# Performance work log

Hardware: AMD Instinct MI355X
Metric: run time of the kernel (lower is better)

The kernel has to match this reference:

```python
import jax, jax.numpy as jnp
import numpy as np

B = 8                                   # point clouds per batch
NS = [65536, 16384, 4096, 1024, 256]    # points per scale (stride-4 downsampling)
CS = [32, 64, 128, 256, 512]            # encoder channels per scale
K = 3
BN_EPS = 1e-5


def setup_inputs() -> dict:
    key = jax.random.key(0)
    ks = iter(jax.random.split(key, 64))
    inp = {}
    for i, (n, c) in enumerate(zip(NS, CS)):
        inp[f"p{i}"] = jax.random.uniform(next(ks), (n, 3), jnp.float32)
        inp[f"f{i}"] = jax.random.normal(next(ks), (n, c), jnp.float32)
        inp[f"b{i}"] = jnp.repeat(jnp.arange(B, dtype=jnp.int32), n // B)
    # FP stage mlps: a:(4->3) [768,256,256], b:(3->2) [384,128,128],
    #               c:(2->1) [192,64,64],   d:(1->0) [96,32,32]
    cfg = {"a": (CS[3] + CS[4], CS[3]), "b": (CS[2] + CS[3], CS[2]),
           "c": (CS[1] + CS[2], CS[1]), "d": (CS[0] + CS[1], CS[0])}
    for s, (cin, ch) in cfg.items():
        for j, ci in ((1, cin), (2, ch)):
            inp[f"w{s}{j}"] = jax.random.normal(next(ks), (ci, ch), jnp.float32) / float(np.sqrt(ci))
            inp[f"bias{s}{j}"] = jnp.zeros((ch,), jnp.float32)
            inp[f"g{s}{j}"] = jnp.ones((ch,), jnp.float32)
            inp[f"bt{s}{j}"] = jnp.zeros((ch,), jnp.float32)
    return inp


def _knn_interpolate(x2, p2, p1):
    """torch_geometric.nn.knn_interpolate with k=3; equal-sized sorted batches."""
    n1, n2, c = p1.shape[0] // B, p2.shape[0] // B, x2.shape[1]
    p1b, p2b = p1.reshape(B, n1, 3), p2.reshape(B, n2, 3)
    x2b = x2.reshape(B, n2, c)
    # squared dists via |a|^2 + |b|^2 - 2ab (avoids [B,n1,n2,3] temporary)
    d2 = (jnp.sum(p1b * p1b, -1)[:, :, None] + jnp.sum(p2b * p2b, -1)[:, None, :]
          - 2.0 * jnp.einsum('bnd,bmd->bnm', p1b, p2b))
    neg_d2, idx = jax.lax.top_k(-d2, K)              # [B, n1, K]
    w = 1.0 / jnp.maximum(-neg_d2, 1e-16)            # inverse squared distance
    gath = jax.vmap(lambda x, i: x[i])(x2b, idx)     # [B, n1, K, c]
    out = jnp.einsum('bnk,bnkc->bnc', w, gath) / jnp.sum(w, -1, keepdims=True)
    return out.reshape(B * n1, c)


def _lin_bn_relu(x, w, bias, gamma, beta):
    h = x @ w + bias
    mu = jnp.mean(h, 0)
    var = jnp.mean((h - mu) ** 2, 0)
    return jax.nn.relu((h - mu) * jax.lax.rsqrt(var + BN_EPS) * gamma + beta)


def _fp_stage(p_fine, f_fine, p_coarse, f_coarse, w1, b1, g1, bt1, w2, b2, g2, bt2):
    up = _knn_interpolate(f_coarse, p_coarse, p_fine)
    x = jnp.concatenate([f_fine, up], axis=1)
    x = _lin_bn_relu(x, w1, b1, g1, bt1)
    return _lin_bn_relu(x, w2, b2, g2, bt2)


def reference(p0, p1, p2, p3, p4, f0, f1, f2, f3, f4, b0, b1, b2, b3, b4,
              wa1, biasa1, ga1, bta1, wa2, biasa2, ga2, bta2,
              wb1, biasb1, gb1, btb1, wb2, biasb2, gb2, btb2,
              wc1, biasc1, gc1, btc1, wc2, biasc2, gc2, btc2,
              wd1, biasd1, gd1, btd1, wd2, biasd2, gd2, btd2):
    f3 = _fp_stage(p3, f3, p4, f4, wa1, biasa1, ga1, bta1, wa2, biasa2, ga2, bta2)
    f2 = _fp_stage(p2, f2, p3, f3, wb1, biasb1, gb1, btb1, wb2, biasb2, gb2, btb2)
    f1 = _fp_stage(p1, f1, p2, f2, wc1, biasc1, gc1, btc1, wc2, biasc2, gc2, btc2)
    f0 = _fp_stage(p0, f0, p1, f1, wd1, biasd1, gd1, btd1, wd2, biasd2, gd2, btd2)
    return f0
```

## Files before the change

### kernel.cpp

```cpp
#include <hip/hip_runtime.h>

#define BN_EPS 1e-5f

typedef unsigned short us;

__device__ __forceinline__ float bf2f(us u) {
    union { unsigned int i; float f; } v; v.i = ((unsigned int)u) << 16; return v.f;
}
__device__ __forceinline__ us f2bf(float f) {
    unsigned int x = __float_as_uint(f);
    x += 0x7fffu + ((x >> 16) & 1u);
    return (us)(x >> 16);
}
__device__ __forceinline__ float ldf(const void* p, size_t i, int f32) {
    return f32 ? ((const float*)p)[i] : bf2f(((const us*)p)[i]);
}

__global__ void detect_kernel(const unsigned int* __restrict__ g, int* __restrict__ flag) {
    if (threadIdx.x == 0 && blockIdx.x == 0)
        *flag = ((g[0] & 0xFFFFu) == 0u) ? 1 : 0;
}

__global__ __launch_bounds__(256)
void prep_aos_kernel(const void* __restrict__ p, float4* __restrict__ aos,
                     const int* __restrict__ pf32, int n)
{
    const int i = blockIdx.x * 256 + threadIdx.x;
    if (i >= n) return;
    const int f32 = *pf32;
    const float x = ldf(p, (size_t)3 * i + 0, f32);
    const float y = ldf(p, (size_t)3 * i + 1, f32);
    const float z = ldf(p, (size_t)3 * i + 2, f32);
    const float s2 = __fadd_rn(__fadd_rn(__fmul_rn(x, x), __fmul_rn(y, y)), __fmul_rn(z, z));
    aos[i] = make_float4(__fadd_rn(x, x), __fadd_rn(y, y), __fadd_rn(z, z), s2);
}

template<int NPB>
__global__ __launch_bounds__(NPB / 2)
void sort_aos_kernel(const void* __restrict__ p, const int* __restrict__ pf32,
                     float4* __restrict__ srt, int* __restrict__ jout)
{
    __shared__ float sk[NPB];
    __shared__ int   sj[NPB];
    const int f32 = *pf32;
    const int tid = threadIdx.x;
    const int base = blockIdx.x * NPB;
    for (int i = tid; i < NPB; i += NPB / 2) {
        sk[i] = ldf(p, (size_t)3 * (base + i) + 0, f32);
        sj[i] = i;
    }
    __syncthreads();
    for (int k = 2; k <= NPB; k <<= 1) {
        for (int j = k >> 1; j > 0; j >>= 1) {
            const int i = ((tid / j) * (j << 1)) + (tid % j);
            const int ixj = i + j;
            const bool up = ((i & k) == 0);
            const float a = sk[i], b = sk[ixj];
            const bool sw = up ? (a > b) : (a < b);
            if (sw) {
                sk[i] = b; sk[ixj] = a;
                const int t = sj[i]; sj[i] = sj[ixj]; sj[ixj] = t;
            }
            __syncthreads();
        }
    }
    for (int i = tid; i < NPB; i += NPB / 2) {
        const int jl = sj[i];
        const size_t b = (size_t)3 * (base + jl);
        const float x = ldf(p, b + 0, f32);
        const float y = ldf(p, b + 1, f32);
        const float z = ldf(p, b + 2, f32);
        const float s2 = __fadd_rn(__fadd_rn(__fmul_rn(x, x), __fmul_rn(y, y)),
                                   __fmul_rn(z, z));
        srt[base + i] = make_float4(__fadd_rn(x, x), __fadd_rn(y, y), __fadd_rn(z, z), s2);
        jout[base + i] = base + jl;
    }
}

__device__ __forceinline__ void lexmerge33(
    const float a0, const int A0, const float a1, const int A1, const float a2, const int A2,
    const float b0, const int B0, const float b1, const int B1, const float b2, const int B2,
    float& m0, int& M0, float& m1, int& M1, float& m2, int& M2)
{
    const bool c1 = (a0 < b0) || (a0 == b0 && A0 < B0);
    m0 = c1 ? a0 : b0;  M0 = c1 ? A0 : B0;
    const float hAd = c1 ? a1 : a0;  const int hAi = c1 ? A1 : A0;
    const float hBd = c1 ? b0 : b1;  const int hBi = c1 ? B0 : B1;
    const bool c2 = (hAd < hBd) || (hAd == hBd && hAi < hBi);
    m1 = c2 ? hAd : hBd;  M1 = c2 ? hAi : hBi;
    const float gAd = c2 ? (c1 ? a2 : a1) : hAd;  const int gAi = c2 ? (c1 ? A2 : A1) : hAi;
    const float gBd = c2 ? hBd : (c1 ? b1 : b2);  const int gBi = c2 ? hBi : (c1 ? B1 : B2);
    const bool c3 = (gAd < gBd) || (gAd == gBd && gAi < gBi);
    m2 = c3 ? gAd : gBd;  M2 = c3 ? gAi : gBi;
}

template<int NPB, int C2>
__global__ __launch_bounds__(256)
void knn_win_kernel(const void* __restrict__ p_fine,
                    const float4* __restrict__ srt,
                    const int* __restrict__ jsrt,
                    const float* __restrict__ f_coarse,
                    const float* __restrict__ stats,
                    const void* __restrict__ gamma,
                    const void* __restrict__ beta,
                    float inv_n2,
                    float* __restrict__ up_out,
                    const int* __restrict__ pf32)
{
    __shared__ __align__(16) float4 sA[NPB];
    __shared__ int   sJ[NPB];
    __shared__ float mrg_d[4 * 64 * 3];
    __shared__ int   mrg_i[4 * 64 * 3];
    __shared__ int   s_idx[64][3];
    __shared__ float s_w[64][3];
    __shared__ float aff_a[C2], aff_b[C2];

    const int f32 = *pf32;
    const int tid = threadIdx.x;
    const int lane = tid & 63, wv = tid >> 6;
    const int cb = blockIdx.y * NPB;
    const int row0 = (blockIdx.y * gridDim.x + blockIdx.x) * 64;

    for (int i = tid; i < NPB; i += 256) { sA[i] = srt[cb + i]; sJ[i] = jsrt[cb + i]; }
    for (int c = tid; c < C2; c += 256) {
        const float mu  = stats[c] * inv_n2;
        const float var = stats[C2 + c] * inv_n2 - mu * mu;
        const float a = ldf(gamma, c, f32) * rsqrtf(var + BN_EPS);
        aff_a[c] = a;
        aff_b[c] = ldf(beta, c, f32) - mu * a;
    }
    __syncthreads();

    const int row = row0 + lane;
    const size_t pb = (size_t)row * 3;
    const float px = ldf(p_fine, pb + 0, f32);
    const float py = ldf(p_fine, pb + 1, f32);
    const float pz = ldf(p_fine, pb + 2, f32);
    const float s1 = __fadd_rn(__fadd_rn(__fmul_rn(px, px), __fmul_rn(py, py)),
                               __fmul_rn(pz, pz));
    const float px2 = __fadd_rn(px, px);

    int lo = 0, hi = NPB;
    while (lo < hi) {
        const int mid = (lo + hi) >> 1;
        if (sA[mid].x < px2) lo = mid + 1; else hi = mid;
    }
    const int cpos = lo;

    float t0 = 1e30f, t1 = 1e30f, t2 = 1e30f;
    int i0 = 0, i1 = 0, i2 = 0;

#define WINS(A, D, JJ) {                                                      \
    const bool l0 = (A) && ((D) < t0 || ((D) == t0 && (JJ) < i0));            \
    const bool l1 = (A) && ((D) < t1 || ((D) == t1 && (JJ) < i1));            \
    const bool l2 = (A) && ((D) < t2 || ((D) == t2 && (JJ) < i2));            \
    i2 = l1 ? i1 : (l2 ? (JJ) : i2);                                          \
    i1 = l0 ? i0 : (l1 ? (JJ) : i1);                                          \
    i0 = l0 ? (JJ) : i0;                                                      \
    const float q2 = l1 ? t1 : (l2 ? (D) : t2);                               \
    const float q1 = l0 ? t0 : (l1 ? (D) : t1);                               \
    t0 = l0 ? (D) : t0;  t1 = q1;  t2 = q2; }

    {
        int pos = cpos + wv;
        bool alive = true;
        for (int it = 0; it < NPB / 4 + 2; ++it) {
            if (!__any(alive)) break;
            const bool inb = (pos < NPB);
            const int rp = inb ? pos : (NPB - 1);
            const float4 C = sA[rp];
            const float dq = __fsub_rn(px2, C.x);
            const float dq2 = __fmul_rn(dq, dq);
            alive = alive && inb && !(dq2 > fmaf(4.0f, t2, 4e-5f));
            const float dot2 = fmaf(pz, C.z, fmaf(py, C.y, __fmul_rn(px, C.x)));
            const float d = __fsub_rn(__fadd_rn(s1, C.w), dot2);
            const int jj = sJ[rp];
            WINS(alive, d, jj);
            pos += 4;
        }
    }
    {
        int pos = cpos - 1 - wv;
        bool alive = true;
        for (int it = 0; it < NPB / 4 + 2; ++it) {
            if (!__any(alive)) break;
            const bool inb = (pos >= 0);
            const int rp = inb ? pos : 0;
            const float4 C = sA[rp];
            const float dq = __fsub_rn(px2, C.x);
            const float dq2 = __fmul_rn(dq, dq);
            alive = alive && inb && !(dq2 > fmaf(4.0f, t2, 4e-5f));
            const float dot2 = fmaf(pz, C.z, fmaf(py, C.y, __fmul_rn(px, C.x)));
            const float d = __fsub_rn(__fadd_rn(s1, C.w), dot2);
            const int jj = sJ[rp];
            WINS(alive, d, jj);
            pos -= 4;
        }
    }
#undef WINS

    const int mb = (wv * 64 + lane) * 3;
    mrg_d[mb + 0] = t0;  mrg_i[mb + 0] = i0;
    mrg_d[mb + 1] = t1;  mrg_i[mb + 1] = i1;
    mrg_d[mb + 2] = t2;  mrg_i[mb + 2] = i2;
    __syncthreads();

    if (tid < 64) {
        float d0 = mrg_d[tid * 3 + 0], d1 = mrg_d[tid * 3 + 1], d2 = mrg_d[tid * 3 + 2];
        int   j0 = mrg_i[tid * 3 + 0], j1 = mrg_i[tid * 3 + 1], j2 = mrg_i[tid * 3 + 2];
        #pragma unroll
        for (int w = 1; w < 4; ++w) {
            const int b2 = (w * 64 + tid) * 3;
            float n0, n1, n2v; int ni0, ni1, ni2;
            lexmerge33(d0, j0, d1, j1, d2, j2,
                       mrg_d[b2 + 0], mrg_i[b2 + 0], mrg_d[b2 + 1], mrg_i[b2 + 1],
                       mrg_d[b2 + 2], mrg_i[b2 + 2],
                       n0, ni0, n1, ni1, n2v, ni2);
            d0 = n0; j0 = ni0; d1 = n1; j1 = ni1; d2 = n2v; j2 = ni2;
        }
        s_idx[tid][0] = j0;  s_w[tid][0] = __fdiv_rn(1.0f, fmaxf(d0, 1e-16f));
        s_idx[tid][1] = j1;  s_w[tid][1] = __fdiv_rn(1.0f, fmaxf(d1, 1e-16f));
        s_idx[tid][2] = j2;  s_w[tid][2] = __fdiv_rn(1.0f, fmaxf(d2, 1e-16f));
    }
    __syncthreads();

    for (int p = wv; p < 64; p += 4) {
        const int r2 = row0 + p;
        const int g0 = s_idx[p][0], g1 = s_idx[p][1], g2 = s_idx[p][2];
        const float w0 = s_w[p][0], w1 = s_w[p][1], w2 = s_w[p][2];
        const float den = __fadd_rn(__fadd_rn(w0, w1), w2);
        float* __restrict__ urow = up_out + (size_t)r2 * C2;
        for (int c = lane; c < C2; c += 64) {
            const float aa = aff_a[c], bb = aff_b[c];
            const float v0 = fmaxf(aa * f_coarse[(size_t)g0 * C2 + c] + bb, 0.f);
            const float v1 = fmaxf(aa * f_coarse[(size_t)g1 * C2 + c] + bb, 0.f);
            const float v2 = fmaxf(aa * f_coarse[(size_t)g2 * C2 + c] + bb, 0.f);
            const float num = fmaf(w2, v2, fmaf(w1, v1, __fmul_rn(w0, v0)));
            urow[c] = __fdiv_rn(num, den);
        }
    }
}

template<int MODE, int SPLIT, int LEN>
__global__ __launch_bounds__(64 * SPLIT, 8)
void knn_up_kernel(
    const void* __restrict__ p_fine,
    const float4* __restrict__ aos,
    const void* __restrict__ f_coarse,
    const float* __restrict__ stats,
    const void* __restrict__ gamma,
    const void* __restrict__ beta,
    float inv_n2,
    float* __restrict__ up_out,
    const int* __restrict__ pf32,
    int n2pb, int c2)
{
    __shared__ float mrg_d[SPLIT * 64 * 3];
    __shared__ int   mrg_i[SPLIT * 64 * 3];
    __shared__ float aff_a[256], aff_b[256];
    __shared__ int   s_idx[64][3];
    __shared__ float s_w[64][3];

    const int f32 = *pf32;
    const int tid = threadIdx.x;
    const int lane = tid & 63;
    const int wv = tid >> 6;
    const int cbase = blockIdx.y * n2pb;
    const int row0 = (blockIdx.y * gridDim.x + blockIdx.x) * 64;

    if (MODE == 1) {
        for (int c = tid; c < c2; c += 64 * SPLIT) {
            float mu  = stats[c] * inv_n2;
            float var = stats[c2 + c] * inv_n2 - mu * mu;
            float a = ldf(gamma, c, f32) * rsqrtf(var + BN_EPS);
            aff_a[c] = a;
            aff_b[c] = ldf(beta, c, f32) - mu * a;
        }
    }

    {
        const int row = row0 + lane;
        const size_t b = (size_t)row * 3;
        const float px = ldf(p_fine, b + 0, f32);
        const float py = ldf(p_fine, b + 1, f32);
        const float pz = ldf(p_fine, b + 2, f32);
        const float s1 = __fadd_rn(__fadd_rn(__fmul_rn(px, px), __fmul_rn(py, py)),
                                   __fmul_rn(pz, pz));
        const int jb = wv * LEN;
        unsigned long long spv = (unsigned long long)(const void*)(aos + cbase + jb);
        spv = ((unsigned long long)__builtin_amdgcn_readfirstlane((unsigned int)(spv >> 32)) << 32)
            |  (unsigned long long)__builtin_amdgcn_readfirstlane((unsigned int)spv);
        const float4* __restrict__ sl = (const float4*)spv;

        float t0 = 1e30f, t1 = 1e30f, t2 = 1e30f;
        int i0 = jb, i1 = jb, i2 = jb;

#define KNN_UPD(CQ, JJ) {                                                     \
        const float dot2 = fmaf(pz, (CQ).z, fmaf(py, (CQ).y,                  \
                                __fmul_rn(px, (CQ).x)));                      \
        const float d = __fsub_rn(__fadd_rn(s1, (CQ).w), dot2);               \
        const int jj = (JJ);                                                  \
        const bool a0 = d < t0, a1 = d < t1, a2 = d < t2;                     \
        i2 = a1 ? i1 : (a2 ? jj : i2);                                        \
        i1 = a0 ? i0 : (a1 ? jj : i1);                                        \
        i0 = a0 ? jj : i0;                                                    \
        const float nt1 = __builtin_amdgcn_fmed3f(d, t0, t1);                 \
        const float nt2 = __builtin_amdgcn_fmed3f(d, t1, t2);                 \
        t0 = fminf(d, t0);                                                    \
        t1 = nt1; t2 = nt2; }

        float4 ca = sl[0], cb = sl[1], cc = sl[2], cd = sl[3];
        for (int t = 0; t < LEN; t += 4) {
            float4 na, nb, nc, nd;
            const bool more = (t + 4) < LEN;
            if (more) { na = sl[t + 4]; nb = sl[t + 5]; nc = sl[t + 6]; nd = sl[t + 7]; }
            KNN_UPD(ca, jb + t + 0);
            KNN_UPD(cb, jb + t + 1);
            KNN_UPD(cc, jb + t + 2);
            KNN_UPD(cd, jb + t + 3);
            if (more) { ca = na; cb = nb; cc = nc; cd = nd; }
        }
#undef KNN_UPD

        const int mb = (wv * 64 + lane) * 3;
        mrg_d[mb + 0] = t0;  mrg_i[mb + 0] = cbase + i0;
        mrg_d[mb + 1] = t1;  mrg_i[mb + 1] = cbase + i1;
        mrg_d[mb + 2] = t2;  mrg_i[mb + 2] = cbase + i2;
    }
    __syncthreads();

    if (tid < 64) {
        float d0 = mrg_d[tid * 3 + 0], d1 = mrg_d[tid * 3 + 1], d2 = mrg_d[tid * 3 + 2];
        int   j0 = mrg_i[tid * 3 + 0], j1 = mrg_i[tid * 3 + 1], j2 = mrg_i[tid * 3 + 2];
        #pragma unroll
        for (int w = 1; w < SPLIT; ++w) {
            const int mb = (w * 64 + tid) * 3;
            const float e0 = mrg_d[mb + 0], e1 = mrg_d[mb + 1], e2 = mrg_d[mb + 2];
            const int   k0 = mrg_i[mb + 0], k1 = mrg_i[mb + 1], k2 = mrg_i[mb + 2];
            float n0, n1, n2v; int ni0, ni1, ni2;
            lexmerge33(d0, j0, d1, j1, d2, j2,
                       e0, k0, e1, k1, e2, k2,
                       n0, ni0, n1, ni1, n2v, ni2);
            d0 = n0; j0 = ni0; d1 = n1; j1 = ni1; d2 = n2v; j2 = ni2;
        }
        s_idx[tid][0] = j0;  s_w[tid][0] = __fdiv_rn(1.0f, fmaxf(d0, 1e-16f));
        s_idx[tid][1] = j1;  s_w[tid][1] = __fdiv_rn(1.0f, fmaxf(d1, 1e-16f));
        s_idx[tid][2] = j2;  s_w[tid][2] = __fdiv_rn(1.0f, fmaxf(d2, 1e-16f));
    }
    __syncthreads();

    for (int p = wv; p < 64; p += SPLIT) {
        const int row = row0 + p;
        const int g0 = s_idx[p][0], g1 = s_idx[p][1], g2 = s_idx[p][2];
        const float w0 = s_w[p][0], w1 = s_w[p][1], w2 = s_w[p][2];
        const float den = __fadd_rn(__fadd_rn(w0, w1), w2);
        float* __restrict__ urow = up_out + (size_t)row * c2;
        for (int c = lane; c < c2; c += 64) {
            float v0, v1, v2;
            if (MODE == 0) {
                v0 = ldf(f_coarse, (size_t)g0 * c2 + c, f32);
                v1 = ldf(f_coarse, (size_t)g1 * c2 + c, f32);
                v2 = ldf(f_coarse, (size_t)g2 * c2 + c, f32);
            } else {
                const float* fc = (const float*)f_coarse;
                const float aa = aff_a[c], bb = aff_b[c];
                v0 = fmaxf(aa * fc[(size_t)g0 * c2 + c] + bb, 0.f);
                v1 = fmaxf(aa * fc[(size_t)g1 * c2 + c] + bb, 0.f);
                v2 = fmaxf(aa * fc[(size_t)g2 * c2 + c] + bb, 0.f);
            }
            const float num = fmaf(w2, v2, fmaf(w1, v1, __fmul_rn(w0, v0)));
            urow[c] = __fdiv_rn(num, den);
        }
    }
}

__global__ __launch_bounds__(256)
void gemm1_bn_kernel(const void* __restrict__ Ffine,
                     const float* __restrict__ Up,
                     const void* __restrict__ W,
                     const void* __restrict__ bias,
                     float* __restrict__ H,
                     float* __restrict__ stats_out,
                     const int* __restrict__ pf32,
                     int M, int c1, int c2, int N)
{
    __shared__ __align__(16) float As[16][68];
    __shared__ __align__(16) float Bs[16][68];
    __shared__ float s_sum[64], s_sq[64];

    const int f32 = *pf32;
    const int K = c1 + c2;
    const int tid = threadIdx.x;
    const int tx = tid & 15, ty = tid >> 4;
    const int n0 = blockIdx.x * 64, m0 = blockIdx.y * 64;

    if (tid < 64) { s_sum[tid] = 0.f; s_sq[tid] = 0.f; }

    const int a_m = tid >> 2;
    const int a_k = (tid & 3) << 2;
    const int b_k = tid >> 4;
    const int b_n = (tid & 15) << 2;
    const int row = m0 + a_m;

    float avp[4]; float4 bvp;
    {
        const int k = a_k;
        if (k < c1) {
            if (f32) {
                const float4 v = *(const float4*)((const float*)Ffine + (size_t)row * c1 + k);
                avp[0] = v.x; avp[1] = v.y; avp[2] = v.z; avp[3] = v.w;
            } else {
                const ushort4 u = *(const ushort4*)((const us*)Ffine + (size_t)row * c1 + k);
                avp[0] = bf2f(u.x); avp[1] = bf2f(u.y); avp[2] = bf2f(u.z); avp[3] = bf2f(u.w);
            }
        } else {
            const float4 v = *(const float4*)(Up + (size_t)row * c2 + (k - c1));
            avp[0] = v.x; avp[1] = v.y; avp[2] = v.z; avp[3] = v.w;
        }
        bvp = make_float4(0.f, 0.f, 0.f, 0.f);
        if (n0 + b_n < N) {
            const size_t wi = (size_t)b_k * N + (n0 + b_n);
            if (f32) bvp = *(const float4*)((const float*)W + wi);
            else {
                const ushort4 u = *(const ushort4*)((const us*)W + wi);
                bvp = make_float4(bf2f(u.x), bf2f(u.y), bf2f(u.z), bf2f(u.w));
            }
        }
    }

    float acc[4][4] = {};

    for (int k0 = 0; k0 < K; k0 += 16) {
        #pragma unroll
        for (int i = 0; i < 4; ++i) As[a_k + i][a_m] = avp[i];
        *(float4*)&Bs[b_k][b_n] = bvp;
        __syncthreads();

        float avn[4]; float4 bvn;
        const int kn = k0 + 16;
        if (kn < K) {
            const int k = kn + a_k;
            if (k < c1) {
                if (f32) {
                    const float4 v = *(const float4*)((const float*)Ffine + (size_t)row * c1 + k);
                    avn[0] = v.x; avn[1] = v.y; avn[2] = v.z; avn[3] = v.w;
                } else {
                    const ushort4 u = *(const ushort4*)((const us*)Ffine + (size_t)row * c1 + k);
                    avn[0] = bf2f(u.x); avn[1] = bf2f(u.y); avn[2] = bf2f(u.z); avn[3] = bf2f(u.w);
                }
            } else {
                const float4 v = *(const float4*)(Up + (size_t)row * c2 + (k - c1));
                avn[0] = v.x; avn[1] = v.y; avn[2] = v.z; avn[3] = v.w;
            }
            bvn = make_float4(0.f, 0.f, 0.f, 0.f);
            if (n0 + b_n < N) {
                const size_t wi = (size_t)(kn + b_k) * N + (n0 + b_n);
                if (f32) bvn = *(const float4*)((const float*)W + wi);
                else {
                    const ushort4 u = *(const ushort4*)((const us*)W + wi);
                    bvn = make_float4(bf2f(u.x), bf2f(u.y), bf2f(u.z), bf2f(u.w));
                }
            }
        }

        #pragma unroll
        for (int kk = 0; kk < 16; ++kk) {
            const float4 a4 = *(const float4*)&As[kk][ty << 2];
            const float4 b4 = *(const float4*)&Bs[kk][tx << 2];
            const float aarr[4] = {a4.x, a4.y, a4.z, a4.w};
            const float barr[4] = {b4.x, b4.y, b4.z, b4.w};
            #pragma unroll
            for (int i = 0; i < 4; ++i)
                #pragma unroll
                for (int j = 0; j < 4; ++j)
                    acc[i][j] = fmaf(aarr[i], barr[j], acc[i][j]);
        }
        __syncthreads();

        if (kn < K) {
            #pragma unroll
            for (int i = 0; i < 4; ++i) avp[i] = avn[i];
            bvp = bvn;
        }
    }

    float bvals[4];
    const bool colsok = (n0 + (tx << 2)) < N;
    #pragma unroll
    for (int j = 0; j < 4; ++j) {
        const int n = n0 + (tx << 2) + j;
        bvals[j] = (n < N) ? ldf(bias, n, f32) : 0.f;
    }
    float ps[4] = {0.f, 0.f, 0.f, 0.f}, pq[4] = {0.f, 0.f, 0.f, 0.f};
    #pragma unroll
    for (int i = 0; i < 4; ++i) {
        float4 hv;
        float* hvp = (float*)&hv;
        #pragma unroll
        for (int j = 0; j < 4; ++j) {
            const float v = acc[i][j] + bvals[j];
            hvp[j] = v;
            ps[j] += v;
            pq[j] = fmaf(v, v, pq[j]);
        }
        if (colsok)
            *(float4*)(H + (size_t)(m0 + (ty << 2) + i) * N + n0 + (tx << 2)) = hv;
    }
    #pragma unroll
    for (int j = 0; j < 4; ++j) {
        atomicAdd(&s_sum[(tx << 2) + j], ps[j]);
        atomicAdd(&s_sq[(tx << 2) + j], pq[j]);
    }
    __syncthreads();
    if (tid < 64) {
        const int n = n0 + tid;
        if (n < N) {
            atomicAdd(&stats_out[n], s_sum[tid]);
            atomicAdd(&stats_out[N + n], s_sq[tid]);
        }
    }
}

__global__ __launch_bounds__(256)
void gemm2_bn_kernel(const float* __restrict__ A,
                     const void* __restrict__ W,
                     const void* __restrict__ bias,
                     const float* __restrict__ stats_in,
                     const void* __restrict__ g_in,
                     const void* __restrict__ bt_in,
                     float inv_m,
                     float* __restrict__ H,
                     float* __restrict__ stats_out,
                     const int* __restrict__ pf32,
                     int M, int K, int N)
{
    __shared__ __align__(16) float As[16][68];
    __shared__ __align__(16) float Bs[16][68];
    __shared__ float aff_a[256], aff_b[256];
    __shared__ float s_sum[64], s_sq[64];

    const int f32 = *pf32;
    const int tid = threadIdx.x;
    const int tx = tid & 15, ty = tid >> 4;
    const int n0 = blockIdx.x * 64, m0 = blockIdx.y * 64;

    for (int c = tid; c < K; c += 256) {
        float mu  = stats_in[c] * inv_m;
        float var = stats_in[K + c] * inv_m - mu * mu;
        float a = ldf(g_in, c, f32) * rsqrtf(var + BN_EPS);
        aff_a[c] = a; aff_b[c] = ldf(bt_in, c, f32) - mu * a;
    }
    if (tid < 64) { s_sum[tid] = 0.f; s_sq[tid] = 0.f; }
    __syncthreads();

    const int a_m = tid >> 2;
    const int a_k = (tid & 3) << 2;
    const int b_k = tid >> 4;
    const int b_n = (tid & 15) << 2;
    const int row = m0 + a_m;

    float avp[4]; float4 bvp;
    {
        const float4 af = *(const float4*)(A + (size_t)row * K + a_k);
        avp[0] = af.x; avp[1] = af.y; avp[2] = af.z; avp[3] = af.w;
        bvp = make_float4(0.f, 0.f, 0.f, 0.f);
        if (n0 + b_n < N) {
            const size_t wi = (size_t)b_k * N + (n0 + b_n);
            if (f32) bvp = *(const float4*)((const float*)W + wi);
            else {
                const ushort4 u = *(const ushort4*)((const us*)W + wi);
                bvp = make_float4(bf2f(u.x), bf2f(u.y), bf2f(u.z), bf2f(u.w));
            }
        }
    }

    float acc[4][4] = {};

    for (int k0 = 0; k0 < K; k0 += 16) {
        #pragma unroll
        for (int i = 0; i < 4; ++i)
            As[a_k + i][a_m] = fmaxf(fmaf(aff_a[k0 + a_k + i], avp[i], aff_b[k0 + a_k + i]), 0.f);
        *(float4*)&Bs[b_k][b_n] = bvp;
        __syncthreads();

        float avn[4]; float4 bvn;
        const int kn = k0 + 16;
        if (kn < K) {
            const float4 af = *(const float4*)(A + (size_t)row * K + (kn + a_k));
            avn[0] = af.x; avn[1] = af.y; avn[2] = af.z; avn[3] = af.w;
            bvn = make_float4(0.f, 0.f, 0.f, 0.f);
            if (n0 + b_n < N) {
                const size_t wi = (size_t)(kn + b_k) * N + (n0 + b_n);
                if (f32) bvn = *(const float4*)((const float*)W + wi);
                else {
                    const ushort4 u = *(const ushort4*)((const us*)W + wi);
                    bvn = make_float4(bf2f(u.x), bf2f(u.y), bf2f(u.z), bf2f(u.w));
                }
            }
        }

        #pragma unroll
        for (int kk = 0; kk < 16; ++kk) {
            const float4 a4 = *(const float4*)&As[kk][ty << 2];
            const float4 b4 = *(const float4*)&Bs[kk][tx << 2];
            const float aarr[4] = {a4.x, a4.y, a4.z, a4.w};
            const float barr[4] = {b4.x, b4.y, b4.z, b4.w};
            #pragma unroll
            for (int i = 0; i < 4; ++i)
                #pragma unroll
                for (int j = 0; j < 4; ++j)
                    acc[i][j] = fmaf(aarr[i], barr[j], acc[i][j]);
        }
        __syncthreads();

        if (kn < K) {
            #pragma unroll
            for (int i = 0; i < 4; ++i) avp[i] = avn[i];
            bvp = bvn;
        }
    }

    float bvals[4];
    const bool colsok = (n0 + (tx << 2)) < N;
    #pragma unroll
    for (int j = 0; j < 4; ++j) {
        const int n = n0 + (tx << 2) + j;
        bvals[j] = (n < N) ? ldf(bias, n, f32) : 0.f;
    }
    float ps[4] = {0.f, 0.f, 0.f, 0.f}, pq[4] = {0.f, 0.f, 0.f, 0.f};
    #pragma unroll
    for (int i = 0; i < 4; ++i) {
        float4 hv;
        float* hvp = (float*)&hv;
        #pragma unroll
        for (int j = 0; j < 4; ++j) {
            const float v = acc[i][j] + bvals[j];
            hvp[j] = v;
            ps[j] += v;
            pq[j] = fmaf(v, v, pq[j]);
        }
        if (colsok)
            *(float4*)(H + (size_t)(m0 + (ty << 2) + i) * N + n0 + (tx << 2)) = hv;
    }
    #pragma unroll
    for (int j = 0; j < 4; ++j) {
        atomicAdd(&s_sum[(tx << 2) + j], ps[j]);
        atomicAdd(&s_sq[(tx << 2) + j], pq[j]);
    }
    __syncthreads();
    if (tid < 64) {
        const int n = n0 + tid;
        if (n < N) {
            atomicAdd(&stats_out[n], s_sum[tid]);
            atomicAdd(&stats_out[N + n], s_sq[tid]);
        }
    }
}

__global__ __launch_bounds__(256)
void finalize_kernel(const float* __restrict__ Hf, const float* __restrict__ stats,
                     const void* __restrict__ g, const void* __restrict__ bt,
                     float inv_m, void* __restrict__ out,
                     const int* __restrict__ pf32, int total)
{
    const int idx = blockIdx.x * 256 + threadIdx.x;
    if (idx >= total) return;
    const int f32 = *pf32;
    const int c = idx & 31;
    const float mu  = stats[c] * inv_m;
    const float var = stats[32 + c] * inv_m - mu * mu;
    const float a = ldf(g, c, f32) * rsqrtf(var + BN_EPS);
    const float b = ldf(bt, c, f32) - mu * a;
    const float v = fmaxf(fmaf(a, Hf[idx], b), 0.f);
    if (f32) ((float*)out)[idx] = v;
    else     ((us*)out)[idx] = f2bf(v);
}

extern "C" void kernel_launch(void* const* d_in, const int* in_sizes, int n_in,
                              void* d_out, int out_size, void* d_ws, size_t ws_size,
                              hipStream_t stream) {
    (void)in_sizes; (void)n_in; (void)out_size; (void)ws_size;
    const void* p0 = d_in[0];
    const void* f0 = d_in[1];
    const void* p1 = d_in[3];
    const void* f1 = d_in[4];
    const void* p2 = d_in[6];
    const void* f2 = d_in[7];
    const void* p3 = d_in[9];
    const void* f3 = d_in[10];
    const void* p4 = d_in[12];
    const void* f4 = d_in[13];
    const void *W1[4], *B1[4], *G1[4], *T1[4], *W2[4], *B2[4], *G2[4], *T2[4];
    for (int s = 0; s < 4; ++s) {
        const int b = 15 + s * 8;
        W1[s] = d_in[b + 0]; B1[s] = d_in[b + 1];
        G1[s] = d_in[b + 2]; T1[s] = d_in[b + 3];
        W2[s] = d_in[b + 4]; B2[s] = d_in[b + 5];
        G2[s] = d_in[b + 6]; T2[s] = d_in[b + 7];
    }

    float* stats = (float*)d_ws;
    float* st_a1 = stats + 0;
    float* st_a2 = stats + 512;
    float* st_b1 = stats + 1024;
    float* st_b2 = stats + 1280;
    float* st_c1 = stats + 1536;
    float* st_c2 = stats + 1664;
    float* st_d1 = stats + 1792;
    float* st_d2 = stats + 1856;
    int*   flag  = (int*)(stats + 1920);
    float* U = (float*)((char*)d_ws + 8192);
    float* H = U + 4194304;
    float* h2a = H + 262144;
    float* h2b = H + 524288;
    float* h2c = H + 1048576;
    float* h2d = U;
    float4* aosbuf = (float4*)H;
    float4* srtbuf = (float4*)H;
    int*    jbuf   = (int*)(H + 65536);

    hipMemsetAsync(d_ws, 0, 1920 * sizeof(float), stream);
    detect_kernel<<<1, 64, 0, stream>>>((const unsigned int*)G1[0], flag);

    prep_aos_kernel<<<1, 256, 0, stream>>>(p4, aosbuf, flag, 256);
    knn_up_kernel<0, 8, 4><<<dim3(2, 8), 512, 0, stream>>>(
        p3, aosbuf, f4, nullptr, nullptr, nullptr, 0.f, U, flag, 32, 512);
    gemm1_bn_kernel<<<dim3(4, 16), 256, 0, stream>>>(
        f3, U, W1[0], B1[0], H, st_a1, flag, 1024, 256, 512, 256);
    gemm2_bn_kernel<<<dim3(4, 16), 256, 0, stream>>>(
        H, W2[0], B2[0], st_a1, G1[0], T1[0], 1.f / 1024.f,
        h2a, st_a2, flag, 1024, 256, 256);
    prep_aos_kernel<<<4, 256, 0, stream>>>(p3, aosbuf, flag, 1024);
    knn_up_kernel<1, 8, 16><<<dim3(8, 8), 512, 0, stream>>>(
        p2, aosbuf, h2a, st_a2, G2[0], T2[0], 1.f / 1024.f, U, flag, 128, 256);
    gemm1_bn_kernel<<<dim3(2, 64), 256, 0, stream>>>(
        f2, U, W1[1], B1[1], H, st_b1, flag, 4096, 128, 256, 128);
    gemm2_bn_kernel<<<dim3(2, 64), 256, 0, stream>>>(
        H, W2[1], B2[1], st_b1, G1[1], T1[1], 1.f / 4096.f,
        h2b, st_b2, flag, 4096, 128, 128);
    prep_aos_kernel<<<16, 256, 0, stream>>>(p2, aosbuf, flag, 4096);
    knn_up_kernel<1, 16, 32><<<dim3(32, 8), 1024, 0, stream>>>(
        p1, aosbuf, h2b, st_b2, G2[1], T2[1], 1.f / 4096.f, U, flag, 512, 128);
    gemm1_bn_kernel<<<dim3(1, 256), 256, 0, stream>>>(
        f1, U, W1[2], B1[2], H, st_c1, flag, 16384, 64, 128, 64);
    gemm2_bn_kernel<<<dim3(1, 256), 256, 0, stream>>>(
        H, W2[2], B2[2], st_c1, G1[2], T1[2], 1.f / 16384.f,
        h2c, st_c2, flag, 16384, 64, 64);
    sort_aos_kernel<2048><<<8, 1024, 0, stream>>>(p1, flag, srtbuf, jbuf);
    knn_win_kernel<2048, 64><<<dim3(128, 8), 256, 0, stream>>>(
        p0, srtbuf, jbuf, h2c, st_c2, G2[2], T2[2], 1.f / 16384.f, U, flag);
    gemm1_bn_kernel<<<dim3(1, 1024), 256, 0, stream>>>(
        f0, U, W1[3], B1[3], H, st_d1, flag, 65536, 32, 64, 32);
    gemm2_bn_kernel<<<dim3(1, 1024), 256, 0, stream>>>(
        H, W2[3], B2[3], st_d1, G1[3], T1[3], 1.f / 65536.f,
        h2d, st_d2, flag, 65536, 32, 32);
    finalize_kernel<<<(65536 * 32) / 256, 256, 0, stream>>>(
        h2d, st_d2, G2[3], T2[3], 1.f / 65536.f, d_out, flag, 65536 * 32);
}
```

Baseline: 606.6 us.

## Bin fine query points by x so KNN waves scan coherent sorted windows

Adds histogram, prefix and scatter kernels that bucket the 65536 fine points into 128 x-bins per batch, then a new KNN kernel processes groups of 64 spatially coherent queries per wave. Each wave starts its scan from the minimum query x (a shared start position), and the forward and backward scans are split across two waves instead of four. The goal is to cut wave divergence in the window scan, where before the whole wave kept iterating until its slowest lane finished. The cost is three extra small kernel launches plus a memset, atomics, and scattered output rows.

```diff
diff --git a/kernel.cpp b/kernel.cpp
--- a/kernel.cpp
+++ b/kernel.cpp
@@ -77,6 +77,45 @@
     }
 }
 
+__global__ __launch_bounds__(256)
+void hist_kernel(const void* __restrict__ p, int* __restrict__ hist,
+                 const int* __restrict__ pf32, int nf, int nfpb)
+{
+    const int i = blockIdx.x * 256 + threadIdx.x;
+    if (i >= nf) return;
+    const float x = ldf(p, (size_t)3 * i, *pf32);
+    int bin = (int)(x * 128.0f);
+    bin = bin < 0 ? 0 : (bin > 127 ? 127 : bin);
+    atomicAdd(&hist[(i / nfpb) * 128 + bin], 1);
+}
+
+__global__ __launch_bounds__(64)
+void prefix_kernel(const int* __restrict__ hist, int* __restrict__ cnt)
+{
+    const int b = threadIdx.x;
+    if (b >= 8) return;
+    int acc = 0;
+    for (int i = 0; i < 128; ++i) {
+        cnt[b * 128 + i] = acc;
+        acc += hist[b * 128 + i];
+    }
+}
+
+__global__ __launch_bounds__(256)
+void scatter_kernel(const void* __restrict__ p, int* __restrict__ cnt,
+                    int* __restrict__ qidx, const int* __restrict__ pf32,
+                    int nf, int nfpb)
+{
+    const int i = blockIdx.x * 256 + threadIdx.x;
+    if (i >= nf) return;
+    const float x = ldf(p, (size_t)3 * i, *pf32);
+    int bin = (int)(x * 128.0f);
+    bin = bin < 0 ? 0 : (bin > 127 ? 127 : bin);
+    const int b = i / nfpb;
+    const int pos = atomicAdd(&cnt[b * 128 + bin], 1);
+    qidx[b * nfpb + pos] = i;
+}
+
 __device__ __forceinline__ void lexmerge33(
     const float a0, const int A0, const float a1, const int A1, const float a2, const int A2,
     const float b0, const int B0, const float b1, const int B1, const float b2, const int B2,
@@ -94,35 +133,41 @@
     m2 = c3 ? gAd : gBd;  M2 = c3 ? gAi : gBi;
 }
 
-template<int NPB, int C2>
-__global__ __launch_bounds__(256)
-void knn_win_kernel(const void* __restrict__ p_fine,
-                    const float4* __restrict__ srt,
-                    const int* __restrict__ jsrt,
-                    const float* __restrict__ f_coarse,
-                    const float* __restrict__ stats,
-                    const void* __restrict__ gamma,
-                    const void* __restrict__ beta,
-                    float inv_n2,
-                    float* __restrict__ up_out,
-                    const int* __restrict__ pf32)
+template<int NPB, int C2, int QPB>
+__global__ __launch_bounds__(512)
+void knn_win2_kernel(const void* __restrict__ p_fine,
+                     const float4* __restrict__ srt,
+                     const int* __restrict__ jsrt,
+                     const int* __restrict__ qidx,
+                     const float* __restrict__ f_coarse,
+                     const float* __restrict__ stats,
+                     const void* __restrict__ gamma,
+                     const void* __restrict__ beta,
+                     float inv_n2,
+                     float* __restrict__ up_out,
+                     const int* __restrict__ pf32,
+                     int nfpb)
 {
     __shared__ __align__(16) float4 sA[NPB];
     __shared__ int   sJ[NPB];
-    __shared__ float mrg_d[4 * 64 * 3];
-    __shared__ int   mrg_i[4 * 64 * 3];
-    __shared__ int   s_idx[64][3];
-    __shared__ float s_w[64][3];
+    __shared__ float mrg_d[2 * QPB * 3];
+    __shared__ int   mrg_i[2 * QPB * 3];
+    __shared__ int   s_idx[QPB][3];
+    __shared__ float s_w[QPB][3];
+    __shared__ int   s_qrow[QPB];
     __shared__ float aff_a[C2], aff_b[C2];
 
     const int f32 = *pf32;
     const int tid = threadIdx.x;
-    const int lane = tid & 63, wv = tid >> 6;
+    const int lane = tid & 63;
+    const int wv = tid >> 6;
+    const int g = wv >> 1;
+    const int sp = wv & 1;
     const int cb = blockIdx.y * NPB;
-    const int row0 = (blockIdx.y * gridDim.x + blockIdx.x) * 64;
-
-    for (int i = tid; i < NPB; i += 256) { sA[i] = srt[cb + i]; sJ[i] = jsrt[cb + i]; }
-    for (int c = tid; c < C2; c += 256) {
+
+    for (int i = tid; i < NPB; i += 512) { sA[i] = srt[cb + i]; sJ[i] = jsrt[cb + i]; }
+    if (tid < QPB) s_qrow[tid] = qidx[blockIdx.y * nfpb + blockIdx.x * QPB + tid];
+    for (int c = tid; c < C2; c += 512) {
         const float mu  = stats[c] * inv_n2;
         const float var = stats[C2 + c] * inv_n2 - mu * mu;
         const float a = ldf(gamma, c, f32) * rsqrtf(var + BN_EPS);
@@ -131,8 +176,8 @@
     }
     __syncthreads();
 
-    const int row = row0 + lane;
-    const size_t pb = (size_t)row * 3;
+    const int qrow = s_qrow[g * 64 + lane];
+    const size_t pb = (size_t)qrow * 3;
     const float px = ldf(p_fine, pb + 0, f32);
     const float py = ldf(p_fine, pb + 1, f32);
     const float pz = ldf(p_fine, pb + 2, f32);
@@ -140,20 +185,23 @@
                                __fmul_rn(pz, pz));
     const float px2 = __fadd_rn(px, px);
 
+    float pmn = px2;
+    #pragma unroll
+    for (int m = 1; m < 64; m <<= 1) pmn = fminf(pmn, __shfl_xor(pmn, m, 64));
     int lo = 0, hi = NPB;
     while (lo < hi) {
         const int mid = (lo + hi) >> 1;
-        if (sA[mid].x < px2) lo = mid + 1; else hi = mid;
-    }
-    const int cpos = lo;
+        if (sA[mid].x < pmn) lo = mid + 1; else hi = mid;
+    }
+    const int S = lo;
 
     float t0 = 1e30f, t1 = 1e30f, t2 = 1e30f;
     int i0 = 0, i1 = 0, i2 = 0;
 
-#define WINS(A, D, JJ) {                                                      \
-    const bool l0 = (A) && ((D) < t0 || ((D) == t0 && (JJ) < i0));            \
-    const bool l1 = (A) && ((D) < t1 || ((D) == t1 && (JJ) < i1));            \
-    const bool l2 = (A) && ((D) < t2 || ((D) == t2 && (JJ) < i2));            \
+#define LEXINS(D, JJ) {                                                       \
+    const bool l0 = (D) < t0 || ((D) == t0 && (JJ) < i0);                     \
+    const bool l1 = (D) < t1 || ((D) == t1 && (JJ) < i1);                     \
+    const bool l2 = (D) < t2 || ((D) == t2 && (JJ) < i2);                     \
     i2 = l1 ? i1 : (l2 ? (JJ) : i2);                                          \
     i1 = l0 ? i0 : (l1 ? (JJ) : i1);                                          \
     i0 = l0 ? (JJ) : i0;                                                      \
@@ -162,74 +210,59 @@
     t0 = l0 ? (D) : t0;  t1 = q1;  t2 = q2; }
 
     {
-        int pos = cpos + wv;
         bool alive = true;
-        for (int it = 0; it < NPB / 4 + 2; ++it) {
+        for (int p = S + sp; p < NPB; p += 2) {
             if (!__any(alive)) break;
-            const bool inb = (pos < NPB);
-            const int rp = inb ? pos : (NPB - 1);
-            const float4 C = sA[rp];
+            const float4 C = sA[p];
             const float dq = __fsub_rn(px2, C.x);
             const float dq2 = __fmul_rn(dq, dq);
-            alive = alive && inb && !(dq2 > fmaf(4.0f, t2, 4e-5f));
             const float dot2 = fmaf(pz, C.z, fmaf(py, C.y, __fmul_rn(px, C.x)));
             const float d = __fsub_rn(__fadd_rn(s1, C.w), dot2);
-            const int jj = sJ[rp];
-            WINS(alive, d, jj);
-            pos += 4;
+            LEXINS(d, sJ[p]);
+            alive = alive && !((C.x > px2) && (dq2 > fmaf(4.0f, t2, 4e-5f)));
         }
     }
     {
-        int pos = cpos - 1 - wv;
         bool alive = true;
-        for (int it = 0; it < NPB / 4 + 2; ++it) {
+        for (int p = S - 1 - sp; p >= 0; p -= 2) {
             if (!__any(alive)) break;
-            const bool inb = (pos >= 0);
-            const int rp = inb ? pos : 0;
-            const float4 C = sA[rp];
+            const float4 C = sA[p];
             const float dq = __fsub_rn(px2, C.x);
             const float dq2 = __fmul_rn(dq, dq);
-            alive = alive && inb && !(dq2 > fmaf(4.0f, t2, 4e-5f));
             const float dot2 = fmaf(pz, C.z, fmaf(py, C.y, __fmul_rn(px, C.x)));
             const float d = __fsub_rn(__fadd_rn(s1, C.w), dot2);
-            const int jj = sJ[rp];
-            WINS(alive, d, jj);
-            pos -= 4;
-        }
-    }
-#undef WINS
-
-    const int mb = (wv * 64 + lane) * 3;
+            LEXINS(d, sJ[p]);
+            alive = alive && !(dq2 > fmaf(4.0f, t2, 4e-5f));
+        }
+    }
+#undef LEXINS
+
+    const int mb = (sp * QPB + g * 64 + lane) * 3;
     mrg_d[mb + 0] = t0;  mrg_i[mb + 0] = i0;
     mrg_d[mb + 1] = t1;  mrg_i[mb + 1] = i1;
     mrg_d[mb + 2] = t2;  mrg_i[mb + 2] = i2;
     __syncthreads();
 
-    if (tid < 64) {
-        float d0 = mrg_d[tid * 3 + 0], d1 = mrg_d[tid * 3 + 1], d2 = mrg_d[tid * 3 + 2];
-        int   j0 = mrg_i[tid * 3 + 0], j1 = mrg_i[tid * 3 + 1], j2 = mrg_i[tid * 3 + 2];
-        #pragma unroll
-        for (int w = 1; w < 4; ++w) {
-            const int b2 = (w * 64 + tid) * 3;
-            float n0, n1, n2v; int ni0, ni1, ni2;
-            lexmerge33(d0, j0, d1, j1, d2, j2,
-                       mrg_d[b2 + 0], mrg_i[b2 + 0], mrg_d[b2 + 1], mrg_i[b2 + 1],
-                       mrg_d[b2 + 2], mrg_i[b2 + 2],
-                       n0, ni0, n1, ni1, n2v, ni2);
-            d0 = n0; j0 = ni0; d1 = n1; j1 = ni1; d2 = n2v; j2 = ni2;
-        }
+    if (tid < QPB) {
+        const int a = tid * 3, b = (QPB + tid) * 3;
+        float d0, d1, d2; int j0, j1, j2;
+        lexmerge33(mrg_d[a + 0], mrg_i[a + 0], mrg_d[a + 1], mrg_i[a + 1],
+                   mrg_d[a + 2], mrg_i[a + 2],
+                   mrg_d[b + 0], mrg_i[b + 0], mrg_d[b + 1], mrg_i[b + 1],
+                   mrg_d[b + 2], mrg_i[b + 2],
+                   d0, j0, d1, j1, d2, j2);
         s_idx[tid][0] = j0;  s_w[tid][0] = __fdiv_rn(1.0f, fmaxf(d0, 1e-16f));
         s_idx[tid][1] = j1;  s_w[tid][1] = __fdiv_rn(1.0f, fmaxf(d1, 1e-16f));
         s_idx[tid][2] = j2;  s_w[tid][2] = __fdiv_rn(1.0f, fmaxf(d2, 1e-16f));
     }
     __syncthreads();
 
-    for (int p = wv; p < 64; p += 4) {
-        const int r2 = row0 + p;
+    for (int p = wv; p < QPB; p += 8) {
+        const int row = s_qrow[p];
         const int g0 = s_idx[p][0], g1 = s_idx[p][1], g2 = s_idx[p][2];
         const float w0 = s_w[p][0], w1 = s_w[p][1], w2 = s_w[p][2];
         const float den = __fadd_rn(__fadd_rn(w0, w1), w2);
-        float* __restrict__ urow = up_out + (size_t)r2 * C2;
+        float* __restrict__ urow = up_out + (size_t)row * C2;
         for (int c = lane; c < C2; c += 64) {
             const float aa = aff_a[c], bb = aff_b[c];
             const float v0 = fmaxf(aa * f_coarse[(size_t)g0 * C2 + c] + bb, 0.f);
@@ -718,6 +751,9 @@
     float4* aosbuf = (float4*)H;
     float4* srtbuf = (float4*)H;
     int*    jbuf   = (int*)(H + 65536);
+    int*    qidxbuf = (int*)(H + 81920);
+    int*    histbuf = (int*)(H + 147456);
+    int*    cntbuf  = (int*)(H + 148480);
 
     hipMemsetAsync(d_ws, 0, 1920 * sizeof(float), stream);
     detect_kernel<<<1, 64, 0, stream>>>((const unsigned int*)G1[0], flag);
@@ -747,8 +783,13 @@
         H, W2[2], B2[2], st_c1, G1[2], T1[2], 1.f / 16384.f,
         h2c, st_c2, flag, 16384, 64, 64);
     sort_aos_kernel<2048><<<8, 1024, 0, stream>>>(p1, flag, srtbuf, jbuf);
-    knn_win_kernel<2048, 64><<<dim3(128, 8), 256, 0, stream>>>(
-        p0, srtbuf, jbuf, h2c, st_c2, G2[2], T2[2], 1.f / 16384.f, U, flag);
+    hipMemsetAsync(histbuf, 0, 1024 * sizeof(int), stream);
+    hist_kernel<<<256, 256, 0, stream>>>(p0, histbuf, flag, 65536, 8192);
+    prefix_kernel<<<1, 64, 0, stream>>>(histbuf, cntbuf);
+    scatter_kernel<<<256, 256, 0, stream>>>(p0, cntbuf, qidxbuf, flag, 65536, 8192);
+    knn_win2_kernel<2048, 64, 256><<<dim3(32, 8), 512, 0, stream>>>(
+        p0, srtbuf, jbuf, qidxbuf, h2c, st_c2, G2[2], T2[2],
+        1.f / 16384.f, U, flag, 8192);
     gemm1_bn_kernel<<<dim3(1, 1024), 256, 0, stream>>>(
         f0, U, W1[3], B1[3], H, st_d1, flag, 65536, 32, 64, 32);
     gemm2_bn_kernel<<<dim3(1, 1024), 256, 0, stream>>>(
```

After: 640.7 us. 5.6% more time.
